# Kernel tuning notes

Measured on AMD Instinct MI355X. Metric: run time of the kernel, lower is better.

Reference implementation:

```python
import jax, jax.numpy as jnp
import numpy as np
import math

B, Q, K, C, H, D = 4, 2048, 2048, 128, 8, 16  # c_q=c_k=c_v=C, c_hidden=D, no_heads=H


def setup_inputs() -> dict:
    key = jax.random.key(0)
    k1, k2, k3, k4, k5 = jax.random.split(key, 5)
    return {
        "q_x": jax.random.normal(k1, (B, Q, C), dtype=jnp.float32),
        "kv_x": jax.random.normal(k2, (B, K, C), dtype=jnp.float32),
        # torch Linear weight layout [out_features, in_features] = [H*D, C]
        "w_q": jax.random.normal(k3, (H * D, C), dtype=jnp.float32) * (1.0 / math.sqrt(C)),
        "w_k": jax.random.normal(k4, (H * D, C), dtype=jnp.float32) * (1.0 / math.sqrt(C)),
        "w_v": jax.random.normal(k5, (H * D, C), dtype=jnp.float32) * (1.0 / math.sqrt(C)),
    }


def reference(q_x, kv_x, w_q, w_k, w_v):
    # project + split heads: [B, S, C] x [H, D, C] -> [B, H, S, D]
    wq = w_q.reshape(H, D, C)
    wk = w_k.reshape(H, D, C)
    wv = w_v.reshape(H, D, C)
    q = jnp.einsum("bqc,hdc->bhqd", q_x, wq) / math.sqrt(D)
    k = jnp.einsum("bkc,hdc->bhkd", kv_x, wk)
    v = jnp.einsum("bkc,hdc->bhkd", kv_x, wv)
    scores = jnp.einsum("bhqd,bhkd->bhqk", q, k)  # [B, H, Q, K]
    a = jax.nn.softmax(scores, axis=-1)
    o = jnp.einsum("bhqk,bhkd->bqhd", a, v)  # transpose(-2,-3) -> [B, Q, H, D]
    return o
```

## Files before the change

kernel.cpp:

```cpp
#include <hip/hip_runtime.h>

constexpr int NB   = 4;
constexpr int SEQ  = 2048;
constexpr int CDIM = 128;
constexpr int NH   = 8;
constexpr int HD   = 16;

typedef _Float16 h_t;
typedef __attribute__((ext_vector_type(4))) _Float16 h4;
typedef __attribute__((ext_vector_type(8))) _Float16 h8;
typedef __attribute__((ext_vector_type(2))) __fp16   fp2;
typedef __attribute__((ext_vector_type(4))) float    f4;

constexpr float LOG2E = 1.44269504f;
constexpr float BIAS  = -8.0f * LOG2E;

__global__ __launch_bounds__(256)
void proj(const float* __restrict__ qx, const float* __restrict__ kvx,
          const float* __restrict__ wq, const float* __restrict__ wk,
          const float* __restrict__ wv,
          h_t* __restrict__ qh, h_t* __restrict__ kh, h_t* __restrict__ vF)
{
    const int mat = blockIdx.y;
    const int mb  = blockIdx.x * 64;
    const int wv_ = threadIdx.x >> 6;
    const int ln  = threadIdx.x & 63;
    const int r   = ln & 15, kg = ln >> 4;
    const int stile = mb + wv_ * 16;
    const int srow  = stile + r;

    const float* x = (mat == 0) ? qx : kvx;
    const float* w = (mat == 0) ? wq : (mat == 1) ? wk : wv;
    h_t*         o = (mat == 0) ? qh : (mat == 1) ? kh : vF;
    const float ws_ = (mat == 0) ? 0.25f * LOG2E : 1.0f;

    h8 xf[4];
    #pragma unroll
    for (int kc = 0; kc < 4; ++kc) {
        const float* xp = x + (size_t)srow * CDIM + kc * 32 + kg * 8;
        f4 x0 = *(const f4*)xp;
        f4 x1 = *(const f4*)(xp + 4);
        h8 tf;
        #pragma unroll
        for (int i = 0; i < 4; ++i) { tf[i] = (h_t)x0[i]; tf[4 + i] = (h_t)x1[i]; }
        xf[kc] = tf;
    }

    const int b_ = srow >> 11;
    const int s  = srow & (SEQ - 1);

    #pragma unroll
    for (int nt = 0; nt < 8; ++nt) {
        f4 acc = {0.f, 0.f, 0.f, 0.f};
        #pragma unroll
        for (int kc = 0; kc < 4; ++kc) {
            const float* wp = w + (size_t)(nt * 16 + r) * CDIM + kc * 32 + kg * 8;
            f4 w0 = *(const f4*)wp;
            f4 w1 = *(const f4*)(wp + 4);
            h8 wf;
            #pragma unroll
            for (int i = 0; i < 4; ++i) {
                wf[i]     = (h_t)(w0[i] * ws_);
                wf[4 + i] = (h_t)(w1[i] * ws_);
            }
            acc = (mat == 2)
                ? __builtin_amdgcn_mfma_f32_16x16x32_f16(xf[kc], wf, acc, 0, 0, 0)
                : __builtin_amdgcn_mfma_f32_16x16x32_f16(wf, xf[kc], acc, 0, 0, 0);
        }
        h4 pk;
        #pragma unroll
        for (int i = 0; i < 4; ++i) pk[i] = (h_t)acc[i];

        if (mat == 2) {
            const int bv = stile >> 11, sv = stile & (SEQ - 1);
            *(h4*)(o + (((size_t)bv * NH + nt) * 128 + (sv >> 4)) * 256 + r * 16 + 4 * kg) = pk;
        } else {
            *(h4*)(o + (((size_t)b_ * NH + nt) * SEQ + s) * HD + 4 * kg) = pk;
        }
    }
}

__global__ __launch_bounds__(512, 8)
void attn(const h_t* __restrict__ qh, const h_t* __restrict__ kh,
          const h_t* __restrict__ vF, float* __restrict__ out)
{
    const int bh  = blockIdx.y;
    const int w   = threadIdx.x >> 6;
    const int ws  = w & 3;
    const int kvh = w >> 2;
    const int ln  = threadIdx.x & 63;
    const int r   = ln & 15, kg = ln >> 4;

    __shared__ float oL[4][16][17];
    __shared__ float lL[4][16];

    const size_t hb = (size_t)bh * SEQ * HD;
    const int qb = blockIdx.x * 64 + ws * 16;

    h4 qf = *(const h4*)(qh + hb + (size_t)(qb + r) * HD + kg * 4);

    const h_t* kp = kh + hb + kvh * 64 * 256 + r * HD + kg * 4;
    const h_t* vp = vF + hb + kvh * 64 * 256 + r * 16 + kg * 4;

    float l = 0.f;
    f4 o = {0.f, 0.f, 0.f, 0.f};
    const f4 cbias = {BIAS, BIAS, BIAS, BIAS};

    h4 kfa = *(const h4*)(kp);
    h4 vfa = *(const h4*)(vp);
    h4 kfb = *(const h4*)(kp + 256);
    h4 vfb = *(const h4*)(vp + 256);

    for (int c = 0; c < 64; c += 2) {
        h4 kfn0 = *(const h4*)(kp + (c + 2) * 256);
        h4 vfn0 = *(const h4*)(vp + (c + 2) * 256);
        h4 kfn1 = *(const h4*)(kp + (c + 3) * 256);
        h4 vfn1 = *(const h4*)(vp + (c + 3) * 256);

        {
            f4 s = __builtin_amdgcn_mfma_f32_16x16x16f16(kfa, qf, cbias, 0, 0, 0);
            const float e0 = __builtin_amdgcn_exp2f(s[0]);
            const float e1 = __builtin_amdgcn_exp2f(s[1]);
            const float e2 = __builtin_amdgcn_exp2f(s[2]);
            const float e3 = __builtin_amdgcn_exp2f(s[3]);
            l += (e0 + e1) + (e2 + e3);
            union { fp2 cc[2]; h4 v; } p;
            p.cc[0] = __builtin_amdgcn_cvt_pkrtz(e0, e1);
            p.cc[1] = __builtin_amdgcn_cvt_pkrtz(e2, e3);
            o = __builtin_amdgcn_mfma_f32_16x16x16f16(p.v, vfa, o, 0, 0, 0);
        }
        {
            f4 s = __builtin_amdgcn_mfma_f32_16x16x16f16(kfb, qf, cbias, 0, 0, 0);
            const float e0 = __builtin_amdgcn_exp2f(s[0]);
            const float e1 = __builtin_amdgcn_exp2f(s[1]);
            const float e2 = __builtin_amdgcn_exp2f(s[2]);
            const float e3 = __builtin_amdgcn_exp2f(s[3]);
            l += (e0 + e1) + (e2 + e3);
            union { fp2 cc[2]; h4 v; } p;
            p.cc[0] = __builtin_amdgcn_cvt_pkrtz(e0, e1);
            p.cc[1] = __builtin_amdgcn_cvt_pkrtz(e2, e3);
            o = __builtin_amdgcn_mfma_f32_16x16x16f16(p.v, vfb, o, 0, 0, 0);
        }

        kfa = kfn0; vfa = vfn0;
        kfb = kfn1; vfb = vfn1;
    }

    l += __shfl_xor(l, 16);
    l += __shfl_xor(l, 32);

    if (kvh == 1) {
        #pragma unroll
        for (int reg = 0; reg < 4; ++reg)
            oL[ws][4 * kg + reg][r] = o[reg];
        if (ln < 16) lL[ws][r] = l;
    }
    __syncthreads();

    if (kvh == 0) {
        #pragma unroll
        for (int reg = 0; reg < 4; ++reg)
            o[reg] += oL[ws][4 * kg + reg][r];
        l += lL[ws][r];
        const float inv = 1.f / l;

        const int b_ = bh >> 3, h = bh & 7;
        #pragma unroll
        for (int reg = 0; reg < 4; ++reg) {
            const float iv = __shfl(inv, 4 * kg + reg);
            const int q = qb + 4 * kg + reg;
            out[(((size_t)b_ * SEQ + q) * NH + h) * HD + r] = o[reg] * iv;
        }
    }
}

extern "C" void kernel_launch(void* const* d_in, const int* in_sizes, int n_in,
                              void* d_out, int out_size, void* d_ws, size_t ws_size,
                              hipStream_t stream) {
    const float* qx  = (const float*)d_in[0];
    const float* kvx = (const float*)d_in[1];
    const float* wq  = (const float*)d_in[2];
    const float* wk  = (const float*)d_in[3];
    const float* wv  = (const float*)d_in[4];
    float* out = (float*)d_out;

    const size_t per = (size_t)NB * NH * SEQ * HD;
    h_t* qp = (h_t*)d_ws;
    h_t* kp = qp + per;
    h_t* vp = kp + per;

    proj<<<dim3(128, 3), dim3(256), 0, stream>>>(qx, kvx, wq, wk, wv, qp, kp, vp);
    attn<<<dim3(32, 32), dim3(512), 0, stream>>>(qp, kp, vp, out);
}
```

Measured before the change: 113.6 us.

## Process two query tiles per wave and compute row sums with MFMA

Each wave now handles 32 query rows as two 16-row tiles, so every K/V fragment loaded from global memory is reused twice and the grid is halved. The per-lane scalar row-sum accumulation is replaced by an extra MFMA against a vector of ones, which gives the softmax denominator already in the output layout and removes the shuffles. The cost is more MFMA work per key block (ones products), more registers per thread, and a lower occupancy hint in launch_bounds.

Measured after the change: 104.2 us. -8.3%, faster.

```diff
diff --git a/kernel.cpp b/kernel.cpp
--- a/kernel.cpp
+++ b/kernel.cpp
@@ -80,7 +80,7 @@
     }
 }
 
-__global__ __launch_bounds__(512, 8)
+__global__ __launch_bounds__(512, 4)
 void attn(const h_t* __restrict__ qh, const h_t* __restrict__ kh,
           const h_t* __restrict__ vF, float* __restrict__ out)
 {
@@ -91,20 +91,22 @@
     const int ln  = threadIdx.x & 63;
     const int r   = ln & 15, kg = ln >> 4;
 
-    __shared__ float oL[4][16][17];
-    __shared__ float lL[4][16];
+    __shared__ float oS[4][2][16][17];
+    __shared__ float lS[4][2][16];
 
     const size_t hb = (size_t)bh * SEQ * HD;
-    const int qb = blockIdx.x * 64 + ws * 16;
-
-    h4 qf = *(const h4*)(qh + hb + (size_t)(qb + r) * HD + kg * 4);
+    const int qb = blockIdx.x * 128 + ws * 32;
+
+    h4 qf0 = *(const h4*)(qh + hb + (size_t)(qb + r)      * HD + kg * 4);
+    h4 qf1 = *(const h4*)(qh + hb + (size_t)(qb + 16 + r) * HD + kg * 4);
 
     const h_t* kp = kh + hb + kvh * 64 * 256 + r * HD + kg * 4;
     const h_t* vp = vF + hb + kvh * 64 * 256 + r * 16 + kg * 4;
 
-    float l = 0.f;
-    f4 o = {0.f, 0.f, 0.f, 0.f};
+    f4 o0  = {0.f, 0.f, 0.f, 0.f}, o1  = {0.f, 0.f, 0.f, 0.f};
+    f4 ol0 = {0.f, 0.f, 0.f, 0.f}, ol1 = {0.f, 0.f, 0.f, 0.f};
     const f4 cbias = {BIAS, BIAS, BIAS, BIAS};
+    const h4 ones  = {(h_t)1.f, (h_t)1.f, (h_t)1.f, (h_t)1.f};
 
     h4 kfa = *(const h4*)(kp);
     h4 vfa = *(const h4*)(vp);
@@ -118,58 +120,81 @@
         h4 vfn1 = *(const h4*)(vp + (c + 3) * 256);
 
         {
-            f4 s = __builtin_amdgcn_mfma_f32_16x16x16f16(kfa, qf, cbias, 0, 0, 0);
-            const float e0 = __builtin_amdgcn_exp2f(s[0]);
-            const float e1 = __builtin_amdgcn_exp2f(s[1]);
-            const float e2 = __builtin_amdgcn_exp2f(s[2]);
-            const float e3 = __builtin_amdgcn_exp2f(s[3]);
-            l += (e0 + e1) + (e2 + e3);
-            union { fp2 cc[2]; h4 v; } p;
-            p.cc[0] = __builtin_amdgcn_cvt_pkrtz(e0, e1);
-            p.cc[1] = __builtin_amdgcn_cvt_pkrtz(e2, e3);
-            o = __builtin_amdgcn_mfma_f32_16x16x16f16(p.v, vfa, o, 0, 0, 0);
+            f4 s0 = __builtin_amdgcn_mfma_f32_16x16x16f16(kfa, qf0, cbias, 0, 0, 0);
+            f4 s1 = __builtin_amdgcn_mfma_f32_16x16x16f16(kfa, qf1, cbias, 0, 0, 0);
+            const float e00 = __builtin_amdgcn_exp2f(s0[0]);
+            const float e01 = __builtin_amdgcn_exp2f(s0[1]);
+            const float e02 = __builtin_amdgcn_exp2f(s0[2]);
+            const float e03 = __builtin_amdgcn_exp2f(s0[3]);
+            const float e10 = __builtin_amdgcn_exp2f(s1[0]);
+            const float e11 = __builtin_amdgcn_exp2f(s1[1]);
+            const float e12 = __builtin_amdgcn_exp2f(s1[2]);
+            const float e13 = __builtin_amdgcn_exp2f(s1[3]);
+            union { fp2 cc[2]; h4 v; } p0, p1;
+            p0.cc[0] = __builtin_amdgcn_cvt_pkrtz(e00, e01);
+            p0.cc[1] = __builtin_amdgcn_cvt_pkrtz(e02, e03);
+            p1.cc[0] = __builtin_amdgcn_cvt_pkrtz(e10, e11);
+            p1.cc[1] = __builtin_amdgcn_cvt_pkrtz(e12, e13);
+            o0  = __builtin_amdgcn_mfma_f32_16x16x16f16(p0.v, vfa,  o0,  0, 0, 0);
+            ol0 = __builtin_amdgcn_mfma_f32_16x16x16f16(p0.v, ones, ol0, 0, 0, 0);
+            o1  = __builtin_amdgcn_mfma_f32_16x16x16f16(p1.v, vfa,  o1,  0, 0, 0);
+            ol1 = __builtin_amdgcn_mfma_f32_16x16x16f16(p1.v, ones, ol1, 0, 0, 0);
         }
         {
-            f4 s = __builtin_amdgcn_mfma_f32_16x16x16f16(kfb, qf, cbias, 0, 0, 0);
-            const float e0 = __builtin_amdgcn_exp2f(s[0]);
-            const float e1 = __builtin_amdgcn_exp2f(s[1]);
-            const float e2 = __builtin_amdgcn_exp2f(s[2]);
-            const float e3 = __builtin_amdgcn_exp2f(s[3]);
-            l += (e0 + e1) + (e2 + e3);
-            union { fp2 cc[2]; h4 v; } p;
-            p.cc[0] = __builtin_amdgcn_cvt_pkrtz(e0, e1);
-            p.cc[1] = __builtin_amdgcn_cvt_pkrtz(e2, e3);
-            o = __builtin_amdgcn_mfma_f32_16x16x16f16(p.v, vfb, o, 0, 0, 0);
+            f4 s0 = __builtin_amdgcn_mfma_f32_16x16x16f16(kfb, qf0, cbias, 0, 0, 0);
+            f4 s1 = __builtin_amdgcn_mfma_f32_16x16x16f16(kfb, qf1, cbias, 0, 0, 0);
+            const float e00 = __builtin_amdgcn_exp2f(s0[0]);
+            const float e01 = __builtin_amdgcn_exp2f(s0[1]);
+            const float e02 = __builtin_amdgcn_exp2f(s0[2]);
+            const float e03 = __builtin_amdgcn_exp2f(s0[3]);
+            const float e10 = __builtin_amdgcn_exp2f(s1[0]);
+            const float e11 = __builtin_amdgcn_exp2f(s1[1]);
+            const float e12 = __builtin_amdgcn_exp2f(s1[2]);
+            const float e13 = __builtin_amdgcn_exp2f(s1[3]);
+            union { fp2 cc[2]; h4 v; } p0, p1;
+            p0.cc[0] = __builtin_amdgcn_cvt_pkrtz(e00, e01);
+            p0.cc[1] = __builtin_amdgcn_cvt_pkrtz(e02, e03);
+            p1.cc[0] = __builtin_amdgcn_cvt_pkrtz(e10, e11);
+            p1.cc[1] = __builtin_amdgcn_cvt_pkrtz(e12, e13);
+            o0  = __builtin_amdgcn_mfma_f32_16x16x16f16(p0.v, vfb,  o0,  0, 0, 0);
+            ol0 = __builtin_amdgcn_mfma_f32_16x16x16f16(p0.v, ones, ol0, 0, 0, 0);
+            o1  = __builtin_amdgcn_mfma_f32_16x16x16f16(p1.v, vfb,  o1,  0, 0, 0);
+            ol1 = __builtin_amdgcn_mfma_f32_16x16x16f16(p1.v, ones, ol1, 0, 0, 0);
         }
 
         kfa = kfn0; vfa = vfn0;
         kfb = kfn1; vfb = vfn1;
     }
 
-    l += __shfl_xor(l, 16);
-    l += __shfl_xor(l, 32);
-
     if (kvh == 1) {
         #pragma unroll
-        for (int reg = 0; reg < 4; ++reg)
-            oL[ws][4 * kg + reg][r] = o[reg];
-        if (ln < 16) lL[ws][r] = l;
+        for (int reg = 0; reg < 4; ++reg) {
+            oS[ws][0][4 * kg + reg][r] = o0[reg];
+            oS[ws][1][4 * kg + reg][r] = o1[reg];
+        }
+        if (r == 0) {
+            #pragma unroll
+            for (int reg = 0; reg < 4; ++reg) {
+                lS[ws][0][4 * kg + reg] = ol0[reg];
+                lS[ws][1][4 * kg + reg] = ol1[reg];
+            }
+        }
     }
     __syncthreads();
 
     if (kvh == 0) {
-        #pragma unroll
-        for (int reg = 0; reg < 4; ++reg)
-            o[reg] += oL[ws][4 * kg + reg][r];
-        l += lL[ws][r];
-        const float inv = 1.f / l;
-
         const int b_ = bh >> 3, h = bh & 7;
         #pragma unroll
         for (int reg = 0; reg < 4; ++reg) {
-            const float iv = __shfl(inv, 4 * kg + reg);
-            const int q = qb + 4 * kg + reg;
-            out[(((size_t)b_ * SEQ + q) * NH + h) * HD + r] = o[reg] * iv;
+            const int row = 4 * kg + reg;
+            const float O0 = o0[reg] + oS[ws][0][row][r];
+            const float O1 = o1[reg] + oS[ws][1][row][r];
+            const float L0 = ol0[reg] + lS[ws][0][row];
+            const float L1 = ol1[reg] + lS[ws][1][row];
+            const int q0 = qb + row;
+            const int q1 = q0 + 16;
+            out[(((size_t)b_ * SEQ + q0) * NH + h) * HD + r] = O0 / L0;
+            out[(((size_t)b_ * SEQ + q1) * NH + h) * HD + r] = O1 / L1;
         }
     }
 }
@@ -190,5 +215,5 @@
     h_t* vp = kp + per;
 
     proj<<<dim3(128, 3), dim3(256), 0, stream>>>(qx, kvx, wq, wk, wv, qp, kp, vp);
-    attn<<<dim3(32, 32), dim3(512), 0, stream>>>(qp, kp, vp, out);
+    attn<<<dim3(16, 32), dim3(512), 0, stream>>>(qp, kp, vp, out);
 }
```

## Reuse K/V fragments across four query tiles per wave and compute row sums via MFMA

Applied to the files above, without the earlier changes.

Each wave now holds four 16-row query tiles and reuses every loaded K/V fragment across them, so K/V global loads are amortized over more query work. The key range is split four ways across waves instead of two, and the partials are reduced through shared memory. The softmax denominator is accumulated with an extra MFMA against a ones vector instead of VALU adds and shuffles. The grid is halved, and the launch bound drops to 4 waves per SIMD, which risks lower occupancy and adds matrix-core work.

Measured after the change: 103.9 us. -8.6%, faster.

```diff
diff --git a/kernel.cpp b/kernel.cpp
--- a/kernel.cpp
+++ b/kernel.cpp
@@ -80,96 +80,109 @@
     }
 }
 
-__global__ __launch_bounds__(512, 8)
+__device__ __forceinline__ void chunk4(const h4 kf, const h4 vf,
+                                       const h4* qf, const f4& cbias,
+                                       const h4& ones, f4* o, f4* ol)
+{
+    #pragma unroll
+    for (int j = 0; j < 4; ++j) {
+        f4 s = __builtin_amdgcn_mfma_f32_16x16x16f16(kf, qf[j], cbias, 0, 0, 0);
+        const float e0 = __builtin_amdgcn_exp2f(s[0]);
+        const float e1 = __builtin_amdgcn_exp2f(s[1]);
+        const float e2 = __builtin_amdgcn_exp2f(s[2]);
+        const float e3 = __builtin_amdgcn_exp2f(s[3]);
+        union { fp2 cc[2]; h4 v; } p;
+        p.cc[0] = __builtin_amdgcn_cvt_pkrtz(e0, e1);
+        p.cc[1] = __builtin_amdgcn_cvt_pkrtz(e2, e3);
+        o[j]  = __builtin_amdgcn_mfma_f32_16x16x16f16(p.v, vf,   o[j],  0, 0, 0);
+        ol[j] = __builtin_amdgcn_mfma_f32_16x16x16f16(p.v, ones, ol[j], 0, 0, 0);
+    }
+}
+
+__global__ __launch_bounds__(512, 4)
 void attn(const h_t* __restrict__ qh, const h_t* __restrict__ kh,
           const h_t* __restrict__ vF, float* __restrict__ out)
 {
     const int bh  = blockIdx.y;
     const int w   = threadIdx.x >> 6;
-    const int ws  = w & 3;
-    const int kvh = w >> 2;
+    const int qs  = w & 1;
+    const int kvq = w >> 1;
     const int ln  = threadIdx.x & 63;
     const int r   = ln & 15, kg = ln >> 4;
 
-    __shared__ float oL[4][16][17];
-    __shared__ float lL[4][16];
+    __shared__ float oS[2][3][4][16][17];
+    __shared__ float lS[2][3][4][16];
 
     const size_t hb = (size_t)bh * SEQ * HD;
-    const int qb = blockIdx.x * 64 + ws * 16;
-
-    h4 qf = *(const h4*)(qh + hb + (size_t)(qb + r) * HD + kg * 4);
-
-    const h_t* kp = kh + hb + kvh * 64 * 256 + r * HD + kg * 4;
-    const h_t* vp = vF + hb + kvh * 64 * 256 + r * 16 + kg * 4;
-
-    float l = 0.f;
-    f4 o = {0.f, 0.f, 0.f, 0.f};
+    const int qb = blockIdx.x * 128 + qs * 64;
+
+    h4 qf[4];
+    #pragma unroll
+    for (int j = 0; j < 4; ++j)
+        qf[j] = *(const h4*)(qh + hb + (size_t)(qb + 16 * j + r) * HD + kg * 4);
+
+    const h_t* kp = kh + hb + kvq * 32 * 256 + r * HD + kg * 4;
+    const h_t* vp = vF + hb + kvq * 32 * 256 + r * 16 + kg * 4;
+
+    f4 o[4], ol[4];
+    #pragma unroll
+    for (int j = 0; j < 4; ++j) {
+        o[j]  = (f4){0.f, 0.f, 0.f, 0.f};
+        ol[j] = (f4){0.f, 0.f, 0.f, 0.f};
+    }
     const f4 cbias = {BIAS, BIAS, BIAS, BIAS};
+    const h4 ones  = {(h_t)1.f, (h_t)1.f, (h_t)1.f, (h_t)1.f};
 
     h4 kfa = *(const h4*)(kp);
     h4 vfa = *(const h4*)(vp);
     h4 kfb = *(const h4*)(kp + 256);
     h4 vfb = *(const h4*)(vp + 256);
 
-    for (int c = 0; c < 64; c += 2) {
+    for (int c = 0; c < 32; c += 2) {
         h4 kfn0 = *(const h4*)(kp + (c + 2) * 256);
         h4 vfn0 = *(const h4*)(vp + (c + 2) * 256);
         h4 kfn1 = *(const h4*)(kp + (c + 3) * 256);
         h4 vfn1 = *(const h4*)(vp + (c + 3) * 256);
 
-        {
-            f4 s = __builtin_amdgcn_mfma_f32_16x16x16f16(kfa, qf, cbias, 0, 0, 0);
-            const float e0 = __builtin_amdgcn_exp2f(s[0]);
-            const float e1 = __builtin_amdgcn_exp2f(s[1]);
-            const float e2 = __builtin_amdgcn_exp2f(s[2]);
-            const float e3 = __builtin_amdgcn_exp2f(s[3]);
-            l += (e0 + e1) + (e2 + e3);
-            union { fp2 cc[2]; h4 v; } p;
-            p.cc[0] = __builtin_amdgcn_cvt_pkrtz(e0, e1);
-            p.cc[1] = __builtin_amdgcn_cvt_pkrtz(e2, e3);
-            o = __builtin_amdgcn_mfma_f32_16x16x16f16(p.v, vfa, o, 0, 0, 0);
-        }
-        {
-            f4 s = __builtin_amdgcn_mfma_f32_16x16x16f16(kfb, qf, cbias, 0, 0, 0);
-            const float e0 = __builtin_amdgcn_exp2f(s[0]);
-            const float e1 = __builtin_amdgcn_exp2f(s[1]);
-            const float e2 = __builtin_amdgcn_exp2f(s[2]);
-            const float e3 = __builtin_amdgcn_exp2f(s[3]);
-            l += (e0 + e1) + (e2 + e3);
-            union { fp2 cc[2]; h4 v; } p;
-            p.cc[0] = __builtin_amdgcn_cvt_pkrtz(e0, e1);
-            p.cc[1] = __builtin_amdgcn_cvt_pkrtz(e2, e3);
-            o = __builtin_amdgcn_mfma_f32_16x16x16f16(p.v, vfb, o, 0, 0, 0);
-        }
+        chunk4(kfa, vfa, qf, cbias, ones, o, ol);
+        chunk4(kfb, vfb, qf, cbias, ones, o, ol);
 
         kfa = kfn0; vfa = vfn0;
         kfb = kfn1; vfb = vfn1;
     }
 
-    l += __shfl_xor(l, 16);
-    l += __shfl_xor(l, 32);
-
-    if (kvh == 1) {
-        #pragma unroll
-        for (int reg = 0; reg < 4; ++reg)
-            oL[ws][4 * kg + reg][r] = o[reg];
-        if (ln < 16) lL[ws][r] = l;
+    if (kvq != 0) {
+        const int slot = kvq - 1;
+        #pragma unroll
+        for (int j = 0; j < 4; ++j) {
+            #pragma unroll
+            for (int reg = 0; reg < 4; ++reg)
+                oS[qs][slot][j][4 * kg + reg][r] = o[j][reg];
+            if (r == 0) {
+                #pragma unroll
+                for (int reg = 0; reg < 4; ++reg)
+                    lS[qs][slot][j][4 * kg + reg] = ol[j][reg];
+            }
+        }
     }
     __syncthreads();
 
-    if (kvh == 0) {
-        #pragma unroll
-        for (int reg = 0; reg < 4; ++reg)
-            o[reg] += oL[ws][4 * kg + reg][r];
-        l += lL[ws][r];
-        const float inv = 1.f / l;
-
+    if (kvq == 0) {
         const int b_ = bh >> 3, h = bh & 7;
         #pragma unroll
-        for (int reg = 0; reg < 4; ++reg) {
-            const float iv = __shfl(inv, 4 * kg + reg);
-            const int q = qb + 4 * kg + reg;
-            out[(((size_t)b_ * SEQ + q) * NH + h) * HD + r] = o[reg] * iv;
+        for (int j = 0; j < 4; ++j) {
+            #pragma unroll
+            for (int reg = 0; reg < 4; ++reg) {
+                const int row = 4 * kg + reg;
+                float O = o[j][reg], L = ol[j][reg];
+                #pragma unroll
+                for (int sl = 0; sl < 3; ++sl) {
+                    O += oS[qs][sl][j][row][r];
+                    L += lS[qs][sl][j][row];
+                }
+                const int q = qb + 16 * j + row;
+                out[(((size_t)b_ * SEQ + q) * NH + h) * HD + r] = O / L;
+            }
         }
     }
 }
@@ -190,5 +203,5 @@
     h_t* vp = kp + per;
 
     proj<<<dim3(128, 3), dim3(256), 0, stream>>>(qx, kvx, wq, wk, wv, qp, kp, vp);
-    attn<<<dim3(32, 32), dim3(512), 0, stream>>>(qp, kp, vp, out);
-}
+    attn<<<dim3(16, 32), dim3(512), 0, stream>>>(qp, kp, vp, out);
+}
```
